# Kernel optimization log

Hardware: AMD Instinct MI355X
Metric: run time of the kernel (lower is better)

The kernel has to match this reference:

```python
import jax, jax.numpy as jnp
import numpy as np

B, T, I, H = 128, 64, 128, 256
UNFOLDS = 6
EPS = 1e-08


def setup_inputs() -> dict:
    key = jax.random.key(0)
    ks = jax.random.split(key, 12)
    u = lambda k, sh, lo, hi: jax.random.uniform(k, sh, minval=lo, maxval=hi, dtype=jnp.float32)
    return {
        "x": jax.random.normal(ks[0], (B, T, I), dtype=jnp.float32),
        "input_weight": jnp.ones((I,), jnp.float32),
        "input_bias": jnp.zeros((I,), jnp.float32),
        "sensing_mu": u(ks[1], (I, H), 0.3, 0.8),
        "sensing_sigma": u(ks[2], (I, H), 3.0, 8.0),
        "sensing_w": u(ks[3], (I, H), 0.01, 1.0),
        "sensing_erev": 2.0 * jax.random.randint(ks[4], (I, H), 0, 2).astype(jnp.float32) - 1.0,
        "internal_mu": u(ks[5], (H, H), 0.3, 0.8),
        "internal_sigma": u(ks[6], (H, H), 3.0, 8.0),
        "internal_w": u(ks[7], (H, H), 0.01, 1.0),
        "internal_erev": 2.0 * jax.random.randint(ks[8], (H, H), 0, 2).astype(jnp.float32) - 1.0,
        "vleak": u(ks[9], (H,), -0.2, 0.2),
        "gleak": jnp.ones((H,), jnp.float32),
        "cm": jnp.ones((H,), jnp.float32) * 0.5,
        "output_weight": jnp.ones((H,), jnp.float32),
        "output_bias": jnp.zeros((H,), jnp.float32),
    }


def _gate(V, mu, sigma):
    # torch: sigmoid(sigma * (V.unsqueeze(-1) - mu)); V:[B,D] -> [B,D,H]
    return jax.nn.sigmoid(sigma * (V[..., None] - mu))


def reference(x, input_weight, input_bias, sensing_mu, sensing_sigma, sensing_w,
              sensing_erev, internal_mu, internal_sigma, internal_w, internal_erev,
              vleak, gleak, cm, output_weight, output_bias):
    # time_elapsed = 1.0 default -> cm_t = cm / (1/UNFOLDS) = cm * UNFOLDS
    cm_t = cm * UNFOLDS
    gl_vl = gleak * vleak

    def step(V, xt):
        # affine input mapping
        xm = xt * input_weight + input_bias                      # [B, I]
        s_act = sensing_w * _gate(xm, sensing_mu, sensing_sigma)  # [B, I, H]
        w_num_s = jnp.einsum('bih,ih->bh', s_act, sensing_erev)   # sum over I
        w_den_s = s_act.sum(axis=1)                               # [B, H]

        def unfold(Vc, _):
            w_act = internal_w * _gate(Vc, internal_mu, internal_sigma)  # [B, H, H]
            w_num = jnp.einsum('bij,ij->bj', w_act, internal_erev) + w_num_s
            w_den = w_act.sum(axis=1) + w_den_s
            Vn = (Vc * cm_t + gl_vl + w_num) / (cm_t + gleak + w_den + EPS)
            return Vn, None

        V, _ = jax.lax.scan(unfold, V, None, length=UNFOLDS)
        out_t = V * output_weight + output_bias
        return V, out_t

    h0 = jnp.zeros((x.shape[0], cm.shape[0]), x.dtype)
    hT, out = jax.lax.scan(step, h0, jnp.swapaxes(x, 0, 1))  # scan over T
    return jnp.swapaxes(out, 0, 1), hT  # ([B, T, H], [B, H])
```

## Files before the change

### kernel.cpp

```cpp
#include <hip/hip_runtime.h>
#include <hip/hip_fp16.h>

#define B_ 128
#define T_ 64
#define I_ 128
#define H_ 256
#define UF 6
#define EPSF 1e-8f

typedef _Float16 f16x2 __attribute__((ext_vector_type(2)));
union H2U { __half2 h; f16x2 v; unsigned u; };

static __device__ __forceinline__ float rcpf(float x) { return __builtin_amdgcn_rcpf(x); }
static __device__ __forceinline__ float h2f_lo(unsigned u) {
    return __half2float(__ushort_as_half((unsigned short)(u & 0xffffu)));
}
static __device__ __forceinline__ float h2f_hi(unsigned u) {
    return __half2float(__ushort_as_half((unsigned short)(u >> 16)));
}

__global__ __launch_bounds__(256) void pack_params(
    const float* __restrict__ smu, const float* __restrict__ ssig,
    const float* __restrict__ sw,  const float* __restrict__ serev,
    const float* __restrict__ imu, const float* __restrict__ isig,
    const float* __restrict__ iw,  const float* __restrict__ ierev,
    unsigned* __restrict__ AB_s, unsigned short* __restrict__ WE_s,
    uint2* __restrict__ ABp, unsigned* __restrict__ Wp)
{
    const float L2E = 1.4426950408889634f;
    int idx = blockIdx.x * 256 + threadIdx.x;
    int r = idx >> 8, jg = idx & 255;
    {
        int i0 = 2 * r, i1 = 2 * r + 1;
        unsigned a0 = __half_as_ushort(__float2half_rn(-isig[i0 * H_ + jg] * L2E));
        unsigned a1 = __half_as_ushort(__float2half_rn(-isig[i1 * H_ + jg] * L2E));
        unsigned b0 = __half_as_ushort(__float2half_rn(isig[i0 * H_ + jg] * imu[i0 * H_ + jg] * L2E));
        unsigned b1 = __half_as_ushort(__float2half_rn(isig[i1 * H_ + jg] * imu[i1 * H_ + jg] * L2E));
        ABp[idx] = make_uint2(a0 | (a1 << 16), b0 | (b1 << 16));
        unsigned w0 = __half_as_ushort(__float2half_rn(iw[i0 * H_ + jg] * ierev[i0 * H_ + jg]));
        unsigned w1 = __half_as_ushort(__float2half_rn(iw[i1 * H_ + jg] * ierev[i1 * H_ + jg]));
        Wp[idx] = w0 | (w1 << 16);
    }
    {
        float s = ssig[idx], m = smu[idx];
        unsigned a = __half_as_ushort(__float2half_rn(-s * L2E));
        unsigned b = __half_as_ushort(__float2half_rn(s * m * L2E));
        AB_s[idx] = a | (b << 16);
        WE_s[idx] = __half_as_ushort(__float2half_rn(sw[idx] * serev[idx]));
    }
}

__global__ __launch_bounds__(1024, 4) void ltc_rec(
    const float* __restrict__ x, const float* __restrict__ in_w, const float* __restrict__ in_b,
    const unsigned* __restrict__ AB_s, const unsigned short* __restrict__ WE_s,
    const uint2* __restrict__ ABp, const unsigned* __restrict__ Wp,
    const float* __restrict__ vleak, const float* __restrict__ gleak, const float* __restrict__ cm,
    const float* __restrict__ out_w, const float* __restrict__ out_b,
    unsigned* __restrict__ Vg4,
    float* __restrict__ out, float* __restrict__ hT)
{
    __shared__ unsigned V2u[H_ / 2];
    __shared__ float xs[I_];
    __shared__ float rn[8 * 128], rd[8 * 128];

    const int bx  = blockIdx.x;
    const int b   = bx & 127;
    const int jh  = bx >> 7;
    const int tid = threadIdx.x;
    const int j   = tid & 127;
    const int c   = tid >> 7;
    const int jg  = (jh << 7) + j;
    const int pjbase = ((jh ^ 1) << 7);

    unsigned ra[16], rb[16], rw[16];
    {
        const int po = (jh << 6) + (c << 3);
        const int pp = ((jh ^ 1) << 6) + (c << 3);
        #pragma unroll
        for (int k = 0; k < 8; ++k) {
            uint2 u0 = ABp[((po + k) << 8) + jg];
            ra[k] = u0.x; rb[k] = u0.y; rw[k] = Wp[((po + k) << 8) + jg];
            uint2 u1 = ABp[((pp + k) << 8) + jg];
            ra[8 + k] = u1.x; rb[8 + k] = u1.y; rw[8 + k] = Wp[((pp + k) << 8) + jg];
        }
    }

    float cmt = 0.f, glvl = 0.f, dc = 0.f, owj = 0.f, obj = 0.f, iwv = 0.f, ibv = 0.f;
    if (tid < 128) {
        cmt = cm[jg] * (float)UF;
        float gl = gleak[jg];
        glvl = gl * vleak[jg];
        dc = cmt + gl + EPSF;
        owj = out_w[jg]; obj = out_b[jg];
        iwv = in_w[tid]; ibv = in_b[tid];
    }
    if (tid < H_ / 2) V2u[tid] = 0u;
    float vreg = 0.f;
    __syncthreads();

    const float* xrow = x + (size_t)b * (T_ * I_);
    const __half2 one2 = __float2half2_rn(1.0f);

    for (int t = 0; t < T_; ++t) {
        if (tid < I_) xs[tid] = fmaf(xrow[t * I_ + tid], iwv, ibv);
        __syncthreads();

        float qsn = 0.f, qsd = 0.f;
        {
            const int i0s = c << 4;
            #pragma unroll
            for (int ii = 0; ii < 16; ++ii) {
                const int i = i0s + ii;
                unsigned ab = AB_s[(i << 8) + jg];
                float wv = __half2float(__ushort_as_half(WE_s[(i << 8) + jg]));
                float r  = rcpf(1.f + exp2f(fmaf(h2f_lo(ab), xs[i], h2f_hi(ab))));
                qsn = fmaf(wv, r, qsn);
                qsd = fmaf(fabsf(wv), r, qsd);
            }
        }

        for (int u = 0; u < UF; ++u) {
            const int p = t * UF + u + 1;
            float nm = qsn, dn = qsd;

            {
                const int vb = (jh << 6) + (c << 3);
                #pragma unroll
                for (int k = 0; k < 8; ++k) {
                    H2U v2; v2.u = V2u[vb + k];
                    H2U av; av.u = ra[k];
                    H2U bv; bv.u = rb[k];
                    __half2 z = __hfma2(av.h, v2.h, bv.h);
                    __half2 e = h2exp2(z);
                    __half2 s = __hadd2(e, one2);
                    H2U rv; rv.h = h2rcp(s);
                    H2U ws; ws.u = rw[k];
                    H2U wa; wa.u = ws.u & 0x7fff7fffu;
                    nm = __builtin_amdgcn_fdot2(ws.v, rv.v, nm, false);
                    dn = __builtin_amdgcn_fdot2(wa.v, rv.v, dn, false);
                }
            }

            if (p > 1 && tid < 128) {
                const unsigned* src = Vg4 + (size_t)((p - 1) & 1) * (B_ * H_) + (b << 8) + pjbase + tid;
                unsigned v;
                do { v = __hip_atomic_load(src, __ATOMIC_RELAXED, __HIP_MEMORY_SCOPE_AGENT); }
                while ((v >> 16) != (unsigned)(p - 1));
                unsigned hv = v & 0xffffu;
                unsigned hv1 = (unsigned)__shfl_down((int)hv, 1);
                if (!(tid & 1)) V2u[(pjbase >> 1) + (tid >> 1)] = hv | (hv1 << 16);
            }
            __syncthreads();

            {
                const int vb = ((jh ^ 1) << 6) + (c << 3);
                #pragma unroll
                for (int k = 0; k < 8; ++k) {
                    H2U v2; v2.u = V2u[vb + k];
                    H2U av; av.u = ra[8 + k];
                    H2U bv; bv.u = rb[8 + k];
                    __half2 z = __hfma2(av.h, v2.h, bv.h);
                    __half2 e = h2exp2(z);
                    __half2 s = __hadd2(e, one2);
                    H2U rv; rv.h = h2rcp(s);
                    H2U ws; ws.u = rw[8 + k];
                    H2U wa; wa.u = ws.u & 0x7fff7fffu;
                    nm = __builtin_amdgcn_fdot2(ws.v, rv.v, nm, false);
                    dn = __builtin_amdgcn_fdot2(wa.v, rv.v, dn, false);
                }
            }
            rn[(c << 7) + j] = nm; rd[(c << 7) + j] = dn;
            __syncthreads();

            if (tid < 128) {
                float N = 0.f, D = 0.f;
                #pragma unroll
                for (int k2 = 0; k2 < 8; ++k2) { N += rn[(k2 << 7) + tid]; D += rd[(k2 << 7) + tid]; }
                float Vn = (fmaf(vreg, cmt, glvl) + N) * rcpf(D + dc);
                vreg = Vn;
                unsigned h0 = __half_as_ushort(__float2half_rn(Vn));
                __hip_atomic_store(Vg4 + (size_t)(p & 1) * (B_ * H_) + (b << 8) + jg,
                                   ((unsigned)p << 16) | h0,
                                   __ATOMIC_RELAXED, __HIP_MEMORY_SCOPE_AGENT);
                unsigned h1 = (unsigned)__shfl_down((int)h0, 1);
                if (!(tid & 1)) V2u[jg >> 1] = h0 | (h1 << 16);
                if (u == UF - 1) out[((size_t)b * T_ + t) * H_ + jg] = fmaf(Vn, owj, obj);
            }
            __syncthreads();
        }
    }
    if (tid < 128) hT[(b << 8) + jg] = vreg;
}

extern "C" void kernel_launch(void* const* d_in, const int* in_sizes, int n_in,
                              void* d_out, int out_size, void* d_ws, size_t ws_size,
                              hipStream_t stream) {
    const float* x     = (const float*)d_in[0];
    const float* in_w  = (const float*)d_in[1];
    const float* in_b  = (const float*)d_in[2];
    const float* smu   = (const float*)d_in[3];
    const float* ssig  = (const float*)d_in[4];
    const float* sw    = (const float*)d_in[5];
    const float* serev = (const float*)d_in[6];
    const float* imu   = (const float*)d_in[7];
    const float* isig  = (const float*)d_in[8];
    const float* iw    = (const float*)d_in[9];
    const float* ierev = (const float*)d_in[10];
    const float* vleak = (const float*)d_in[11];
    const float* gleak = (const float*)d_in[12];
    const float* cmv   = (const float*)d_in[13];
    const float* ow    = (const float*)d_in[14];
    const float* ob    = (const float*)d_in[15];

    float* out = (float*)d_out;
    float* hT  = out + (size_t)B_ * T_ * H_;

    char* w = (char*)d_ws;
    uint2*          ABp  = (uint2*)(w);
    unsigned*       Wp   = (unsigned*)(w + (256 << 10));
    unsigned*       AB_s = (unsigned*)(w + (384 << 10));
    unsigned short* WE_s = (unsigned short*)(w + (512 << 10));
    unsigned*       Vg4  = (unsigned*)(w + (576 << 10));

    pack_params<<<dim3(128), dim3(256), 0, stream>>>(
        smu, ssig, sw, serev, imu, isig, iw, ierev, AB_s, WE_s, ABp, Wp);

    ltc_rec<<<dim3(256), dim3(1024), 0, stream>>>(
        x, in_w, in_b, AB_s, WE_s, ABp, Wp, vleak, gleak, cmv, ow, ob,
        Vg4, out, hT);
}
```

Measured before the change: 1.067 ms.

## Remap threads so the K-split reduces via wave shuffles and cache sensing params in registers

Threads are remapped so the 8 partial sums for each output neuron sit in adjacent lanes of one wave. They are reduced with xor shuffles instead of an LDS round trip and an extra block barrier per unfold step. Sensing gate parameters are now packed as half2 pairs and held in registers, and the sensing pass uses packed fp16 exp and rcp. Before this it reloaded fp32-path parameters from global memory every timestep. The pack kernel now zeroes the Vg4 flag buffer, the V and x LDS reads are vectorised to 128-bit, and every thread computes Vn redundantly. Risks include lower fp16 precision in the sensing pass, higher register pressure at 1024 threads, and an uncoalesced per-lane global parameter layout.

```diff
diff --git a/kernel.cpp b/kernel.cpp
--- a/kernel.cpp
+++ b/kernel.cpp
@@ -12,11 +12,19 @@
 union H2U { __half2 h; f16x2 v; unsigned u; };
 
 static __device__ __forceinline__ float rcpf(float x) { return __builtin_amdgcn_rcpf(x); }
-static __device__ __forceinline__ float h2f_lo(unsigned u) {
-    return __half2float(__ushort_as_half((unsigned short)(u & 0xffffu)));
-}
-static __device__ __forceinline__ float h2f_hi(unsigned u) {
-    return __half2float(__ushort_as_half((unsigned short)(u >> 16)));
+
+#define GATE2(VW, AK, BK, WK, NM, DN) {                        \
+    H2U v2_; v2_.u = (VW);                                     \
+    H2U av_; av_.u = (AK);                                     \
+    H2U bv_; bv_.u = (BK);                                     \
+    __half2 z_ = __hfma2(av_.h, v2_.h, bv_.h);                 \
+    __half2 e_ = h2exp2(z_);                                   \
+    __half2 s_ = __hadd2(e_, __float2half2_rn(1.0f));          \
+    H2U rv_; rv_.h = h2rcp(s_);                                \
+    H2U ws_; ws_.u = (WK);                                     \
+    H2U wa_; wa_.u = ws_.u & 0x7fff7fffu;                      \
+    NM = __builtin_amdgcn_fdot2(ws_.v, rv_.v, NM, false);      \
+    DN = __builtin_amdgcn_fdot2(wa_.v, rv_.v, DN, false);      \
 }
 
 __global__ __launch_bounds__(256) void pack_params(
@@ -24,14 +32,15 @@
     const float* __restrict__ sw,  const float* __restrict__ serev,
     const float* __restrict__ imu, const float* __restrict__ isig,
     const float* __restrict__ iw,  const float* __restrict__ ierev,
-    unsigned* __restrict__ AB_s, unsigned short* __restrict__ WE_s,
-    uint2* __restrict__ ABp, unsigned* __restrict__ Wp)
+    uint2* __restrict__ ABp, unsigned* __restrict__ Wp,
+    uint2* __restrict__ SAB, unsigned* __restrict__ SW,
+    unsigned* __restrict__ Vg4)
 {
     const float L2E = 1.4426950408889634f;
     int idx = blockIdx.x * 256 + threadIdx.x;
     int r = idx >> 8, jg = idx & 255;
     {
-        int i0 = 2 * r, i1 = 2 * r + 1;
+        int i0 = 2 * r, i1 = i0 + 1;
         unsigned a0 = __half_as_ushort(__float2half_rn(-isig[i0 * H_ + jg] * L2E));
         unsigned a1 = __half_as_ushort(__float2half_rn(-isig[i1 * H_ + jg] * L2E));
         unsigned b0 = __half_as_ushort(__float2half_rn(isig[i0 * H_ + jg] * imu[i0 * H_ + jg] * L2E));
@@ -41,82 +50,93 @@
         unsigned w1 = __half_as_ushort(__float2half_rn(iw[i1 * H_ + jg] * ierev[i1 * H_ + jg]));
         Wp[idx] = w0 | (w1 << 16);
     }
-    {
-        float s = ssig[idx], m = smu[idx];
-        unsigned a = __half_as_ushort(__float2half_rn(-s * L2E));
-        unsigned b = __half_as_ushort(__float2half_rn(s * m * L2E));
-        AB_s[idx] = a | (b << 16);
-        WE_s[idx] = __half_as_ushort(__float2half_rn(sw[idx] * serev[idx]));
-    }
+    if (idx < 64 * H_) {
+        int i0 = 2 * r, i1 = i0 + 1;
+        unsigned a0 = __half_as_ushort(__float2half_rn(-ssig[i0 * H_ + jg] * L2E));
+        unsigned a1 = __half_as_ushort(__float2half_rn(-ssig[i1 * H_ + jg] * L2E));
+        unsigned b0 = __half_as_ushort(__float2half_rn(ssig[i0 * H_ + jg] * smu[i0 * H_ + jg] * L2E));
+        unsigned b1 = __half_as_ushort(__float2half_rn(ssig[i1 * H_ + jg] * smu[i1 * H_ + jg] * L2E));
+        SAB[idx] = make_uint2(a0 | (a1 << 16), b0 | (b1 << 16));
+        unsigned w0 = __half_as_ushort(__float2half_rn(sw[i0 * H_ + jg] * serev[i0 * H_ + jg]));
+        unsigned w1 = __half_as_ushort(__float2half_rn(sw[i1 * H_ + jg] * serev[i1 * H_ + jg]));
+        SW[idx] = w0 | (w1 << 16);
+    }
+    Vg4[idx] = 0u;
+    Vg4[idx + 32768] = 0u;
 }
 
 __global__ __launch_bounds__(1024, 4) void ltc_rec(
     const float* __restrict__ x, const float* __restrict__ in_w, const float* __restrict__ in_b,
-    const unsigned* __restrict__ AB_s, const unsigned short* __restrict__ WE_s,
     const uint2* __restrict__ ABp, const unsigned* __restrict__ Wp,
+    const uint2* __restrict__ SAB, const unsigned* __restrict__ SW,
     const float* __restrict__ vleak, const float* __restrict__ gleak, const float* __restrict__ cm,
     const float* __restrict__ out_w, const float* __restrict__ out_b,
     unsigned* __restrict__ Vg4,
     float* __restrict__ out, float* __restrict__ hT)
 {
-    __shared__ unsigned V2u[H_ / 2];
-    __shared__ float xs[I_];
-    __shared__ float rn[8 * 128], rd[8 * 128];
+    __shared__ __align__(16) unsigned V2u[H_ / 2];
+    __shared__ __align__(16) unsigned xs2[I_ / 2];
 
     const int bx  = blockIdx.x;
     const int b   = bx & 127;
     const int jh  = bx >> 7;
     const int tid = threadIdx.x;
-    const int j   = tid & 127;
-    const int c   = tid >> 7;
+    const int c   = tid & 7;
+    const int j   = tid >> 3;
     const int jg  = (jh << 7) + j;
     const int pjbase = ((jh ^ 1) << 7);
+    const int BH  = B_ * H_;
 
     unsigned ra[16], rb[16], rw[16];
+    unsigned sa[8], sb[8], sw8[8];
     {
         const int po = (jh << 6) + (c << 3);
         const int pp = ((jh ^ 1) << 6) + (c << 3);
+        const int ps = (c << 3);
         #pragma unroll
         for (int k = 0; k < 8; ++k) {
             uint2 u0 = ABp[((po + k) << 8) + jg];
             ra[k] = u0.x; rb[k] = u0.y; rw[k] = Wp[((po + k) << 8) + jg];
             uint2 u1 = ABp[((pp + k) << 8) + jg];
             ra[8 + k] = u1.x; rb[8 + k] = u1.y; rw[8 + k] = Wp[((pp + k) << 8) + jg];
-        }
-    }
-
-    float cmt = 0.f, glvl = 0.f, dc = 0.f, owj = 0.f, obj = 0.f, iwv = 0.f, ibv = 0.f;
-    if (tid < 128) {
-        cmt = cm[jg] * (float)UF;
-        float gl = gleak[jg];
-        glvl = gl * vleak[jg];
-        dc = cmt + gl + EPSF;
-        owj = out_w[jg]; obj = out_b[jg];
-        iwv = in_w[tid]; ibv = in_b[tid];
-    }
+            uint2 u2 = SAB[((ps + k) << 8) + jg];
+            sa[k] = u2.x; sb[k] = u2.y; sw8[k] = SW[((ps + k) << 8) + jg];
+        }
+    }
+
+    const float cmt  = cm[jg] * (float)UF;
+    const float gl   = gleak[jg];
+    const float glvl = gl * vleak[jg];
+    const float dc   = cmt + gl + EPSF;
+    const float owj  = out_w[jg], obj = out_b[jg];
+    float iw0 = 0.f, iw1 = 0.f, ib0 = 0.f, ib1 = 0.f;
+    if (tid < 64) { iw0 = in_w[2 * tid]; iw1 = in_w[2 * tid + 1];
+                    ib0 = in_b[2 * tid]; ib1 = in_b[2 * tid + 1]; }
     if (tid < H_ / 2) V2u[tid] = 0u;
     float vreg = 0.f;
-    __syncthreads();
 
     const float* xrow = x + (size_t)b * (T_ * I_);
-    const __half2 one2 = __float2half2_rn(1.0f);
 
     for (int t = 0; t < T_; ++t) {
-        if (tid < I_) xs[tid] = fmaf(xrow[t * I_ + tid], iwv, ibv);
+        if (tid < 64) {
+            float2 xv = *reinterpret_cast<const float2*>(xrow + t * I_ + 2 * tid);
+            __half2 hh = __floats2half2_rn(fmaf(xv.x, iw0, ib0), fmaf(xv.y, iw1, ib1));
+            H2U u; u.h = hh; xs2[tid] = u.u;
+        }
         __syncthreads();
 
         float qsn = 0.f, qsd = 0.f;
         {
-            const int i0s = c << 4;
-            #pragma unroll
-            for (int ii = 0; ii < 16; ++ii) {
-                const int i = i0s + ii;
-                unsigned ab = AB_s[(i << 8) + jg];
-                float wv = __half2float(__ushort_as_half(WE_s[(i << 8) + jg]));
-                float r  = rcpf(1.f + exp2f(fmaf(h2f_lo(ab), xs[i], h2f_hi(ab))));
-                qsn = fmaf(wv, r, qsn);
-                qsd = fmaf(fabsf(wv), r, qsd);
-            }
+            const uint4 xa = *reinterpret_cast<const uint4*>(xs2 + (c << 3));
+            const uint4 xb = *reinterpret_cast<const uint4*>(xs2 + (c << 3) + 4);
+            GATE2(xa.x, sa[0], sb[0], sw8[0], qsn, qsd);
+            GATE2(xa.y, sa[1], sb[1], sw8[1], qsn, qsd);
+            GATE2(xa.z, sa[2], sb[2], sw8[2], qsn, qsd);
+            GATE2(xa.w, sa[3], sb[3], sw8[3], qsn, qsd);
+            GATE2(xb.x, sa[4], sb[4], sw8[4], qsn, qsd);
+            GATE2(xb.y, sa[5], sb[5], sw8[5], qsn, qsd);
+            GATE2(xb.z, sa[6], sb[6], sw8[6], qsn, qsd);
+            GATE2(xb.w, sa[7], sb[7], sw8[7], qsn, qsd);
         }
 
         for (int u = 0; u < UF; ++u) {
@@ -125,27 +145,24 @@
 
             {
                 const int vb = (jh << 6) + (c << 3);
-                #pragma unroll
-                for (int k = 0; k < 8; ++k) {
-                    H2U v2; v2.u = V2u[vb + k];
-                    H2U av; av.u = ra[k];
-                    H2U bv; bv.u = rb[k];
-                    __half2 z = __hfma2(av.h, v2.h, bv.h);
-                    __half2 e = h2exp2(z);
-                    __half2 s = __hadd2(e, one2);
-                    H2U rv; rv.h = h2rcp(s);
-                    H2U ws; ws.u = rw[k];
-                    H2U wa; wa.u = ws.u & 0x7fff7fffu;
-                    nm = __builtin_amdgcn_fdot2(ws.v, rv.v, nm, false);
-                    dn = __builtin_amdgcn_fdot2(wa.v, rv.v, dn, false);
-                }
+                const uint4 va = *reinterpret_cast<const uint4*>(V2u + vb);
+                const uint4 vb4 = *reinterpret_cast<const uint4*>(V2u + vb + 4);
+                GATE2(va.x,  ra[0], rb[0], rw[0], nm, dn);
+                GATE2(va.y,  ra[1], rb[1], rw[1], nm, dn);
+                GATE2(va.z,  ra[2], rb[2], rw[2], nm, dn);
+                GATE2(va.w,  ra[3], rb[3], rw[3], nm, dn);
+                GATE2(vb4.x, ra[4], rb[4], rw[4], nm, dn);
+                GATE2(vb4.y, ra[5], rb[5], rw[5], nm, dn);
+                GATE2(vb4.z, ra[6], rb[6], rw[6], nm, dn);
+                GATE2(vb4.w, ra[7], rb[7], rw[7], nm, dn);
             }
 
             if (p > 1 && tid < 128) {
-                const unsigned* src = Vg4 + (size_t)((p - 1) & 1) * (B_ * H_) + (b << 8) + pjbase + tid;
+                const unsigned want = (unsigned)(p - 1);
+                const unsigned* src = Vg4 + (size_t)(want & 1) * BH + (b << 8) + pjbase + tid;
                 unsigned v;
                 do { v = __hip_atomic_load(src, __ATOMIC_RELAXED, __HIP_MEMORY_SCOPE_AGENT); }
-                while ((v >> 16) != (unsigned)(p - 1));
+                while ((v >> 16) != want);
                 unsigned hv = v & 0xffffu;
                 unsigned hv1 = (unsigned)__shfl_down((int)hv, 1);
                 if (!(tid & 1)) V2u[(pjbase >> 1) + (tid >> 1)] = hv | (hv1 << 16);
@@ -154,42 +171,37 @@
 
             {
                 const int vb = ((jh ^ 1) << 6) + (c << 3);
-                #pragma unroll
-                for (int k = 0; k < 8; ++k) {
-                    H2U v2; v2.u = V2u[vb + k];
-                    H2U av; av.u = ra[8 + k];
-                    H2U bv; bv.u = rb[8 + k];
-                    __half2 z = __hfma2(av.h, v2.h, bv.h);
-                    __half2 e = h2exp2(z);
-                    __half2 s = __hadd2(e, one2);
-                    H2U rv; rv.h = h2rcp(s);
-                    H2U ws; ws.u = rw[8 + k];
-                    H2U wa; wa.u = ws.u & 0x7fff7fffu;
-                    nm = __builtin_amdgcn_fdot2(ws.v, rv.v, nm, false);
-                    dn = __builtin_amdgcn_fdot2(wa.v, rv.v, dn, false);
-                }
+                const uint4 va = *reinterpret_cast<const uint4*>(V2u + vb);
+                const uint4 vb4 = *reinterpret_cast<const uint4*>(V2u + vb + 4);
+                GATE2(va.x,  ra[8],  rb[8],  rw[8],  nm, dn);
+                GATE2(va.y,  ra[9],  rb[9],  rw[9],  nm, dn);
+                GATE2(va.z,  ra[10], rb[10], rw[10], nm, dn);
+                GATE2(va.w,  ra[11], rb[11], rw[11], nm, dn);
+                GATE2(vb4.x, ra[12], rb[12], rw[12], nm, dn);
+                GATE2(vb4.y, ra[13], rb[13], rw[13], nm, dn);
+                GATE2(vb4.z, ra[14], rb[14], rw[14], nm, dn);
+                GATE2(vb4.w, ra[15], rb[15], rw[15], nm, dn);
             }
-            rn[(c << 7) + j] = nm; rd[(c << 7) + j] = dn;
-            __syncthreads();
-
-            if (tid < 128) {
-                float N = 0.f, D = 0.f;
-                #pragma unroll
-                for (int k2 = 0; k2 < 8; ++k2) { N += rn[(k2 << 7) + tid]; D += rd[(k2 << 7) + tid]; }
-                float Vn = (fmaf(vreg, cmt, glvl) + N) * rcpf(D + dc);
-                vreg = Vn;
-                unsigned h0 = __half_as_ushort(__float2half_rn(Vn));
-                __hip_atomic_store(Vg4 + (size_t)(p & 1) * (B_ * H_) + (b << 8) + jg,
+
+            nm += __shfl_xor(nm, 1); dn += __shfl_xor(dn, 1);
+            nm += __shfl_xor(nm, 2); dn += __shfl_xor(dn, 2);
+            nm += __shfl_xor(nm, 4); dn += __shfl_xor(dn, 4);
+
+            float Vn = (fmaf(vreg, cmt, glvl) + nm) * rcpf(dn + dc);
+            vreg = Vn;
+            unsigned h0 = __half_as_ushort(__float2half_rn(Vn));
+            if (c == 0)
+                __hip_atomic_store(Vg4 + (size_t)(p & 1) * BH + (b << 8) + jg,
                                    ((unsigned)p << 16) | h0,
                                    __ATOMIC_RELAXED, __HIP_MEMORY_SCOPE_AGENT);
-                unsigned h1 = (unsigned)__shfl_down((int)h0, 1);
-                if (!(tid & 1)) V2u[jg >> 1] = h0 | (h1 << 16);
-                if (u == UF - 1) out[((size_t)b * T_ + t) * H_ + jg] = fmaf(Vn, owj, obj);
-            }
+            unsigned h1 = (unsigned)__shfl_down((int)h0, 8);
+            if (c == 0 && !(j & 1)) V2u[jg >> 1] = h0 | (h1 << 16);
             __syncthreads();
         }
-    }
-    if (tid < 128) hT[(b << 8) + jg] = vreg;
+
+        if (c == 0) out[((size_t)b * T_ + t) * H_ + jg] = fmaf(vreg, owj, obj);
+    }
+    if (c == 0) hT[(b << 8) + jg] = vreg;
 }
 
 extern "C" void kernel_launch(void* const* d_in, const int* in_sizes, int n_in,
@@ -216,16 +228,16 @@
     float* hT  = out + (size_t)B_ * T_ * H_;
 
     char* w = (char*)d_ws;
-    uint2*          ABp  = (uint2*)(w);
-    unsigned*       Wp   = (unsigned*)(w + (256 << 10));
-    unsigned*       AB_s = (unsigned*)(w + (384 << 10));
-    unsigned short* WE_s = (unsigned short*)(w + (512 << 10));
-    unsigned*       Vg4  = (unsigned*)(w + (576 << 10));
+    uint2*    ABp = (uint2*)(w);
+    unsigned* Wp  = (unsigned*)(w + (256 << 10));
+    uint2*    SAB = (uint2*)(w + (384 << 10));
+    unsigned* SW  = (unsigned*)(w + (512 << 10));
+    unsigned* Vg4 = (unsigned*)(w + (576 << 10));
 
     pack_params<<<dim3(128), dim3(256), 0, stream>>>(
-        smu, ssig, sw, serev, imu, isig, iw, ierev, AB_s, WE_s, ABp, Wp);
+        smu, ssig, sw, serev, imu, isig, iw, ierev, ABp, Wp, SAB, SW, Vg4);
 
     ltc_rec<<<dim3(256), dim3(1024), 0, stream>>>(
-        x, in_w, in_b, AB_s, WE_s, ABp, Wp, vleak, gleak, cmv, ow, ob,
+        x, in_w, in_b, ABp, Wp, SAB, SW, vleak, gleak, cmv, ow, ob,
         Vg4, out, hT);
 }
```

After: 1.017 ms. -4.7%, faster.
